# Performance work log

Measured on AMD Instinct MI355X. Metric: run time of the kernel, lower is better.

Reference implementation:

```python
import jax, jax.numpy as jnp
import numpy as np

N_HEADS = 8
NUM_CLASSES = 8
ATTN_INTENSE = 1.0


def setup_inputs() -> dict:
    key = jax.random.key(0)
    k1, k2, k3, k4 = jax.random.split(key, 4)
    bs, width, T = 8, 1536, 1024
    qkv = jax.random.normal(k1, (bs, width, T), dtype=jnp.float32)
    attn_mask = jax.random.randint(k2, (bs, 32, 32), 0, NUM_CLASSES, dtype=jnp.int32)
    # class embedding table: NUM_CLASSES rows + 1 null row (used for the global pass)
    embed_table = jax.random.normal(k3, (NUM_CLASSES + 1, 512), dtype=jnp.float32) * 0.02
    # Conv1d(embed_dim=512 -> 3*ch=192, kernel=1, bias=False) weight
    W_cls = jax.random.normal(k4, (192, 512), dtype=jnp.float32) * 0.02
    return {"qkv": qkv, "attn_mask": attn_mask, "embed_table": embed_table, "W_cls": W_cls}


def _attend(q, k, v, scale):
    # q,k,v: [B, T, C]; returns [B, T, C]
    logits = jnp.einsum('btc,bsc->bts', q * scale, k * scale)
    w = jax.nn.softmax(logits, axis=-1)
    return jnp.einsum('bts,bsc->btc', w, v)


def reference(qkv, attn_mask, embed_table, W_cls):
    bs, width, T = qkv.shape
    H = N_HEADS
    ch = width // (3 * H)            # 64
    scale = ch ** -0.25              # 1/sqrt(sqrt(ch))
    bH = bs * H

    qkv_h = qkv.reshape(bH, 3 * ch, T)
    q = jnp.transpose(qkv_h[:, 0 * ch:1 * ch], (0, 2, 1))  # [bH, T, ch]
    k = jnp.transpose(qkv_h[:, 1 * ch:2 * ch], (0, 2, 1))
    v = jnp.transpose(qkv_h[:, 2 * ch:3 * ch], (0, 2, 1))

    # ---- global pass with null class token ----
    null_tok = W_cls @ embed_table[NUM_CLASSES]  # [3*ch]
    qn, kn, vn = null_tok[:ch], null_tok[ch:2 * ch], null_tok[2 * ch:]
    a = _attend(q + qn, k + kn, v + vn, scale)   # [bH, T, ch]

    # ---- per-region (per segmentation class) attention ----
    seg = attn_mask.reshape(bs, T)
    segs = jnp.repeat(seg, H, axis=0)            # [bH, T], sample-major like qkv reshape

    out = a
    counter = jnp.ones((bH, T), dtype=qkv.dtype)
    for c in range(NUM_CLASSES):
        tok = W_cls @ embed_table[c]             # [3*ch], same token at every region position
        qc, kc, vc = tok[:ch], tok[ch:2 * ch], tok[2 * ch:]
        m = segs == c                            # [bH, T]
        logits = jnp.einsum('btc,bsc->bts', (q + qc) * scale, (k + kc) * scale)
        logits = jnp.where(m[:, None, :], logits, -1e9)   # restrict keys to region
        w = jax.nn.softmax(logits, axis=-1)
        a_c = jnp.einsum('bts,bsc->btc', w, v + vc)
        out = out + jnp.where(m[:, :, None], a_c, 0.0)    # scatter-add onto region queries
        counter = counter + ATTN_INTENSE * m.astype(counter.dtype)

    out = out / counter[:, :, None]              # [bH, T, ch]
    # faithful to original: outs are [ch, T] each, torch.stack(dim=1) -> [ch, bH, T], then reshape
    stacked = jnp.transpose(out, (2, 0, 1))      # [ch, bH, T]
    return stacked.reshape(bs, H * ch, T)
```

## Files before the change

### kernel.cpp

```cpp
#include <hip/hip_runtime.h>
#include <stdint.h>

typedef unsigned short u16;
typedef unsigned int   u32;
typedef __bf16 bf16_t;
typedef bf16_t bf16x8 __attribute__((ext_vector_type(8)));
typedef bf16_t bf16x2 __attribute__((ext_vector_type(2)));
typedef float  f32x2  __attribute__((ext_vector_type(2)));
typedef float  f32x4  __attribute__((ext_vector_type(4)));

#define QSCALE 0.18033688011112042f
#define LP 72

__device__ __forceinline__ u32 pkbf(float a, float b) {
  f32x2 x = {a, b};
  bf16x2 y = __builtin_convertvector(x, bf16x2);
  union { bf16x2 v; u32 u; } c; c.v = y; return c.u;
}

__device__ __forceinline__ float fexp2(float x) {
#if __has_builtin(__builtin_amdgcn_exp2f)
  return __builtin_amdgcn_exp2f(x);
#else
  float r;
  asm("v_exp_f32 %0, %1\n\ts_nop 0" : "=v"(r) : "v"(x));
  return r;
#endif
}

__global__ void tok_kernel(const float* __restrict__ W, const float* __restrict__ E,
                           float* __restrict__ tok) {
  int c = blockIdx.x;
  int j = threadIdx.x;
  const f32x4* wr = (const f32x4*)(W + j * 512);
  const f32x4* er = (const f32x4*)(E + c * 512);
  float acc = 0.f;
  for (int i = 0; i < 128; ++i) {
    f32x4 w = wr[i], e = er[i];
    acc += w.x * e.x + w.y * e.y + w.z * e.z + w.w * e.w;
  }
  tok[c * 192 + j] = acc;
}

__global__ __launch_bounds__(256, 4)
void attn_kernel(const float* __restrict__ qkv, const int* __restrict__ seg,
                 const float* __restrict__ tok, float* __restrict__ out) {
  __shared__ __align__(16) u16 smem[64 * LP * 2 + 4 * 2 * 16 * LP];
  u16* ktr = smem;
  u16* vls = smem + 64 * LP;

  const int L  = blockIdx.x;
  const int bh = (L & 7) * 8 + ((L >> 3) & 7);
  const int qt = L >> 6;
  const int b  = bh >> 3;
  const int tid = threadIdx.x, wave = tid >> 6, lane = tid & 63;
  const int quad = lane >> 4, l16 = lane & 15;
  u16* Pw = smem + 2 * 64 * LP + wave * (2 * 16 * LP);

  const float* qg   = qkv + (size_t)bh * 192 * 1024;
  const int*   segb = seg + b * 1024;

  const int tq = qt * 64 + wave * 16 + l16;
  const int mycls = segb[tq];
  int sq[4];
#pragma unroll
  for (int r = 0; r < 4; ++r) sq[r] = segb[qt * 64 + wave * 16 + quad * 4 + r];

  const float* tn = tok + 8 * 192;
  const float* tc = tok + mycls * 192;
  union { u32 w[4]; bf16x8 v; } q0f[2], qbf[2];
#pragma unroll
  for (int kc = 0; kc < 2; ++kc)
#pragma unroll
    for (int jj = 0; jj < 4; ++jj) {
      int d = kc * 32 + quad * 8 + jj * 2;
      float a0 = qg[(size_t)d * 1024 + tq];
      float a1 = qg[(size_t)(d + 1) * 1024 + tq];
      q0f[kc].w[jj] = pkbf((a0 + tn[d]) * QSCALE, (a1 + tn[d + 1]) * QSCALE);
      qbf[kc].w[jj] = pkbf((a0 + tc[d]) * QSCALE, (a1 + tc[d + 1]) * QSCALE);
    }

  f32x4 O0[4], Ob[4];
#pragma unroll
  for (int dt = 0; dt < 4; ++dt) {
    O0[dt] = (f32x4){0.f, 0.f, 0.f, 0.f};
    Ob[dt] = (f32x4){0.f, 0.f, 0.f, 0.f};
  }
  float rs0[4] = {0.f, 0.f, 0.f, 0.f}, rsb[4] = {0.f, 0.f, 0.f, 0.f};

  const int sK = tid & 63, gK = tid >> 6;
  const int lV = tid & 15, dgV = tid >> 4;
  const float* kbase = qg + (size_t)(64  + gK * 16) * 1024 + sK;
  const float* vbase = qg + (size_t)(128 + dgV * 4) * 1024 + lV;

  for (int kt = 0; kt < 16; ++kt) {
    const int s0 = kt * 64;
    __syncthreads();

    float kf[16];
#pragma unroll
    for (int i = 0; i < 16; ++i) kf[i] = kbase[(size_t)i * 1024 + s0];
    float vf[4][4];
#pragma unroll
    for (int i = 0; i < 4; ++i)
#pragma unroll
      for (int m = 0; m < 4; ++m) vf[i][m] = vbase[(size_t)i * 1024 + s0 + m * 16];

    {
      u32 kp[8];
#pragma unroll
      for (int j = 0; j < 8; ++j) kp[j] = pkbf(kf[2 * j], kf[2 * j + 1]);
      *(uint4*)&ktr[sK * LP + gK * 16]     = make_uint4(kp[0], kp[1], kp[2], kp[3]);
      *(uint4*)&ktr[sK * LP + gK * 16 + 8] = make_uint4(kp[4], kp[5], kp[6], kp[7]);
    }
#pragma unroll
    for (int i = 0; i < 4; ++i)
      *(uint2*)&vls[(dgV * 4 + i) * LP + lV * 4] =
          make_uint2(pkbf(vf[i][0], vf[i][1]), pkbf(vf[i][2], vf[i][3]));

    int sk[4];
#pragma unroll
    for (int n4 = 0; n4 < 4; ++n4) sk[n4] = segb[s0 + n4 * 16 + l16];
    __syncthreads();

    f32x4 S0[4], Sb[4];
#pragma unroll
    for (int n4 = 0; n4 < 4; ++n4) {
      const int scol = n4 * 16 + l16;
      f32x4 a0 = {0.f, 0.f, 0.f, 0.f}, ab = {0.f, 0.f, 0.f, 0.f};
#pragma unroll
      for (int kc = 0; kc < 2; ++kc) {
        bf16x8 kfr = *(const bf16x8*)&ktr[scol * LP + kc * 32 + quad * 8];
        a0 = __builtin_amdgcn_mfma_f32_16x16x32_bf16(q0f[kc].v, kfr, a0, 0, 0, 0);
        ab = __builtin_amdgcn_mfma_f32_16x16x32_bf16(qbf[kc].v, kfr, ab, 0, 0, 0);
      }
      S0[n4] = a0; Sb[n4] = ab;
    }

#pragma unroll
    for (int r = 0; r < 4; ++r) {
      float p0[4], pb[4];
#pragma unroll
      for (int n4 = 0; n4 < 4; ++n4) {
        p0[n4] = fexp2(S0[n4][r]);
        pb[n4] = (sk[n4] == sq[r]) ? fexp2(Sb[n4][r]) : 0.f;
      }
      rs0[r] += (p0[0] + p0[1]) + (p0[2] + p0[3]);
      rsb[r] += (pb[0] + pb[1]) + (pb[2] + pb[3]);
      *(uint2*)&Pw[(quad * 4 + r) * LP + l16 * 4] =
          make_uint2(pkbf(p0[0], p0[1]), pkbf(p0[2], p0[3]));
      *(uint2*)&Pw[16 * LP + (quad * 4 + r) * LP + l16 * 4] =
          make_uint2(pkbf(pb[0], pb[1]), pkbf(pb[2], pb[3]));
    }
    asm volatile("s_waitcnt lgkmcnt(0)" ::: "memory");

#pragma unroll
    for (int kc = 0; kc < 2; ++kc) {
      bf16x8 pf0 = *(const bf16x8*)&Pw[l16 * LP + kc * 32 + quad * 8];
      bf16x8 pfb = *(const bf16x8*)&Pw[16 * LP + l16 * LP + kc * 32 + quad * 8];
#pragma unroll
      for (int dt = 0; dt < 4; ++dt) {
        bf16x8 vfr = *(const bf16x8*)&vls[(dt * 16 + l16) * LP + kc * 32 + quad * 8];
        O0[dt] = __builtin_amdgcn_mfma_f32_16x16x32_bf16(pf0, vfr, O0[dt], 0, 0, 0);
        Ob[dt] = __builtin_amdgcn_mfma_f32_16x16x32_bf16(pfb, vfr, Ob[dt], 0, 0, 0);
      }
    }
  }

#pragma unroll
  for (int r = 0; r < 4; ++r)
#pragma unroll
    for (int off = 1; off < 16; off <<= 1) {
      rs0[r] += __shfl_xor(rs0[r], off, 64);
      rsb[r] += __shfl_xor(rsb[r], off, 64);
    }
  float inv0[4], invb[4];
#pragma unroll
  for (int r = 0; r < 4; ++r) {
    inv0[r] = (rs0[r] > 0.f) ? 1.f / rs0[r] : 0.f;
    invb[r] = (rsb[r] > 0.f) ? 1.f / rsb[r] : 0.f;
  }

  __syncthreads();
  float* fbuf = (float*)smem;
  const float* tvn = tok + 8 * 192 + 128;
#pragma unroll
  for (int dt = 0; dt < 4; ++dt) {
    const int d = dt * 16 + l16;
    const float bn = tvn[d];
#pragma unroll
    for (int r = 0; r < 4; ++r) {
      float bc = tok[sq[r] * 192 + 128 + d];
      float vA = O0[dt][r] * inv0[r] + bn;
      float vB = Ob[dt][r] * invb[r] + bc;
      fbuf[d * 65 + wave * 16 + quad * 4 + r] = 0.5f * (vA + vB);
    }
  }
  __syncthreads();
  {
    const size_t obase = (size_t)bh * 1024 + qt * 64;
    for (int i = tid; i < 4096; i += 256) {
      int d = i >> 6, t = i & 63;
      out[(size_t)d * 65536 + obase + t] = fbuf[d * 65 + t];
    }
  }
}

extern "C" void kernel_launch(void* const* d_in, const int* in_sizes, int n_in,
                              void* d_out, int out_size, void* d_ws, size_t ws_size,
                              hipStream_t stream) {
  (void)in_sizes; (void)n_in; (void)out_size; (void)ws_size;
  const float* qkv   = (const float*)d_in[0];
  const int*   amask = (const int*)d_in[1];
  const float* emb   = (const float*)d_in[2];
  const float* wcls  = (const float*)d_in[3];
  float* tok = (float*)d_ws;
  float* out = (float*)d_out;

  hipLaunchKernelGGL(tok_kernel, dim3(9), dim3(192), 0, stream, wcls, emb, tok);
  hipLaunchKernelGGL(attn_kernel, dim3(1024), dim3(256), 0, stream,
                     qkv, amask, tok, out);
}
```

Baseline: 147.3 us.

## Pre-convert K/V into swizzled bf16 tiles and double-buffer them via async LDS loads

A new prep kernel converts K and V from fp32 to bf16 once per tile and stores them in workspace already laid out with an XOR swizzle. The same launch also computes the class tokens with one wave per output, replacing the old 9-block kernel. The attention kernel now copies each pre-built tile straight into LDS with global_load_lds, double-buffered so the next key tile loads while the current one is computed. This removes the repeated fp32 loads, bf16 conversion and one barrier per iteration, and the swizzle replaces the padded LDS layout. In exchange it adds a 16 MB workspace round-trip, relies on the barrier to wait for the async loads, and lowers the launch-bounds occupancy hint from 4 to 3.

After: 141.2 us. -4.1%, faster.

```diff
diff --git a/kernel.cpp b/kernel.cpp
--- a/kernel.cpp
+++ b/kernel.cpp
@@ -10,7 +10,6 @@
 typedef float  f32x4  __attribute__((ext_vector_type(4)));
 
 #define QSCALE 0.18033688011112042f
-#define LP 72
 
 __device__ __forceinline__ u32 pkbf(float a, float b) {
   f32x2 x = {a, b};
@@ -28,26 +27,75 @@
 #endif
 }
 
-__global__ void tok_kernel(const float* __restrict__ W, const float* __restrict__ E,
-                           float* __restrict__ tok) {
-  int c = blockIdx.x;
-  int j = threadIdx.x;
-  const f32x4* wr = (const f32x4*)(W + j * 512);
-  const f32x4* er = (const f32x4*)(E + c * 512);
-  float acc = 0.f;
-  for (int i = 0; i < 128; ++i) {
-    f32x4 w = wr[i], e = er[i];
-    acc += w.x * e.x + w.y * e.y + w.z * e.z + w.w * e.w;
-  }
-  tok[c * 192 + j] = acc;
-}
-
-__global__ __launch_bounds__(256, 4)
+__device__ __forceinline__ void gload_lds16(const void* g, void* l) {
+  __builtin_amdgcn_global_load_lds(
+      (const __attribute__((address_space(1))) void*)g,
+      (__attribute__((address_space(3))) void*)l, 16, 0, 0);
+}
+
+__global__ __launch_bounds__(256)
+void prep_kernel(const float* __restrict__ qkv,
+                 const float* __restrict__ W, const float* __restrict__ E,
+                 float* __restrict__ tok, u16* __restrict__ tiles) {
+  const int B = blockIdx.x;
+  const int tid = threadIdx.x;
+  if (B >= 1024) {
+    const int gw = (B - 1024) * 4 + (tid >> 6);
+    const int lane = tid & 63;
+    if (gw < 1728) {
+      const int c = gw / 192, j = gw - c * 192;
+      const f32x4* w4 = (const f32x4*)(W + (size_t)j * 512 + lane * 8);
+      const f32x4* e4 = (const f32x4*)(E + (size_t)c * 512 + lane * 8);
+      float acc = 0.f;
+#pragma unroll
+      for (int i = 0; i < 2; ++i) {
+        f32x4 w = w4[i], e = e4[i];
+        acc += w.x * e.x + w.y * e.y + w.z * e.z + w.w * e.w;
+      }
+#pragma unroll
+      for (int off = 32; off; off >>= 1) acc += __shfl_xor(acc, off, 64);
+      if (lane == 0) tok[c * 192 + j] = acc;
+    }
+    return;
+  }
+  const int bh = B >> 4, kt = B & 15;
+  const int s0 = kt * 64;
+  const float* qg = qkv + (size_t)bh * 192 * 1024;
+  u16* img = tiles + (size_t)B * 8192;
+  {
+    const int s = tid & 63, g = tid >> 6;
+    const float* kb = qg + (size_t)(64 + g * 16) * 1024 + s0 + s;
+    float kf[16];
+#pragma unroll
+    for (int i = 0; i < 16; ++i) kf[i] = kb[(size_t)i * 1024];
+    u32 kp[8];
+#pragma unroll
+    for (int j2 = 0; j2 < 8; ++j2) kp[j2] = pkbf(kf[2 * j2], kf[2 * j2 + 1]);
+    const int xr = (s & 7) << 3;
+    *(uint4*)&img[s * 64 + ((g * 16)     ^ xr)] = make_uint4(kp[0], kp[1], kp[2], kp[3]);
+    *(uint4*)&img[s * 64 + ((g * 16 + 8) ^ xr)] = make_uint4(kp[4], kp[5], kp[6], kp[7]);
+  }
+  {
+    const int lV = tid & 15, dg = tid >> 4;
+    const float* vb = qg + (size_t)(128 + dg * 4) * 1024 + s0 + lV;
+#pragma unroll
+    for (int i = 0; i < 4; ++i) {
+      float v0 = vb[(size_t)i * 1024 +  0];
+      float v1 = vb[(size_t)i * 1024 + 16];
+      float v2 = vb[(size_t)i * 1024 + 32];
+      float v3 = vb[(size_t)i * 1024 + 48];
+      const int d = dg * 4 + i;
+      *(uint2*)&img[4096 + d * 64 + ((lV * 4) ^ ((d & 7) << 3))] =
+          make_uint2(pkbf(v0, v1), pkbf(v2, v3));
+    }
+  }
+}
+
+__global__ __launch_bounds__(256, 3)
 void attn_kernel(const float* __restrict__ qkv, const int* __restrict__ seg,
-                 const float* __restrict__ tok, float* __restrict__ out) {
-  __shared__ __align__(16) u16 smem[64 * LP * 2 + 4 * 2 * 16 * LP];
-  u16* ktr = smem;
-  u16* vls = smem + 64 * LP;
+                 const float* __restrict__ tok, const u16* __restrict__ tiles,
+                 float* __restrict__ out) {
+  __shared__ __align__(16) u16 smem[24576];
 
   const int L  = blockIdx.x;
   const int bh = (L & 7) * 8 + ((L >> 3) & 7);
@@ -55,10 +103,11 @@
   const int b  = bh >> 3;
   const int tid = threadIdx.x, wave = tid >> 6, lane = tid & 63;
   const int quad = lane >> 4, l16 = lane & 15;
-  u16* Pw = smem + 2 * 64 * LP + wave * (2 * 16 * LP);
+  u16* Pw = smem + 16384 + wave * 2048;
 
   const float* qg   = qkv + (size_t)bh * 192 * 1024;
   const int*   segb = seg + b * 1024;
+  const u16*   tbh  = tiles + (size_t)bh * (16 * 8192);
 
   const int tq = qt * 64 + wave * 16 + l16;
   const int mycls = segb[tq];
@@ -88,40 +137,31 @@
   }
   float rs0[4] = {0.f, 0.f, 0.f, 0.f}, rsb[4] = {0.f, 0.f, 0.f, 0.f};
 
-  const int sK = tid & 63, gK = tid >> 6;
-  const int lV = tid & 15, dgV = tid >> 4;
-  const float* kbase = qg + (size_t)(64  + gK * 16) * 1024 + sK;
-  const float* vbase = qg + (size_t)(128 + dgV * 4) * 1024 + lV;
-
+  {
+    const char* src = (const char*)tbh + tid * 16;
+    char* dst = (char*)smem + tid * 16;
+#pragma unroll
+    for (int i = 0; i < 4; ++i) gload_lds16(src + i * 4096, dst + i * 4096);
+  }
+
+  const int xq = (l16 & 7) << 3;
+
+#pragma unroll 2
   for (int kt = 0; kt < 16; ++kt) {
     const int s0 = kt * 64;
     __syncthreads();
-
-    float kf[16];
-#pragma unroll
-    for (int i = 0; i < 16; ++i) kf[i] = kbase[(size_t)i * 1024 + s0];
-    float vf[4][4];
-#pragma unroll
-    for (int i = 0; i < 4; ++i)
-#pragma unroll
-      for (int m = 0; m < 4; ++m) vf[i][m] = vbase[(size_t)i * 1024 + s0 + m * 16];
-
-    {
-      u32 kp[8];
-#pragma unroll
-      for (int j = 0; j < 8; ++j) kp[j] = pkbf(kf[2 * j], kf[2 * j + 1]);
-      *(uint4*)&ktr[sK * LP + gK * 16]     = make_uint4(kp[0], kp[1], kp[2], kp[3]);
-      *(uint4*)&ktr[sK * LP + gK * 16 + 8] = make_uint4(kp[4], kp[5], kp[6], kp[7]);
-    }
-#pragma unroll
-    for (int i = 0; i < 4; ++i)
-      *(uint2*)&vls[(dgV * 4 + i) * LP + lV * 4] =
-          make_uint2(pkbf(vf[i][0], vf[i][1]), pkbf(vf[i][2], vf[i][3]));
-
+    if (kt + 1 < 16) {
+      const char* src = (const char*)tbh + (size_t)(kt + 1) * 16384 + tid * 16;
+      char* dst = (char*)smem + ((kt + 1) & 1) * 16384 + tid * 16;
+#pragma unroll
+      for (int i = 0; i < 4; ++i) gload_lds16(src + i * 4096, dst + i * 4096);
+    }
     int sk[4];
 #pragma unroll
     for (int n4 = 0; n4 < 4; ++n4) sk[n4] = segb[s0 + n4 * 16 + l16];
-    __syncthreads();
+
+    const u16* ktr = smem + (kt & 1) * 8192;
+    const u16* vls = ktr + 4096;
 
     f32x4 S0[4], Sb[4];
 #pragma unroll
@@ -130,7 +170,7 @@
       f32x4 a0 = {0.f, 0.f, 0.f, 0.f}, ab = {0.f, 0.f, 0.f, 0.f};
 #pragma unroll
       for (int kc = 0; kc < 2; ++kc) {
-        bf16x8 kfr = *(const bf16x8*)&ktr[scol * LP + kc * 32 + quad * 8];
+        bf16x8 kfr = *(const bf16x8*)&ktr[scol * 64 + ((kc * 32 + quad * 8) ^ xq)];
         a0 = __builtin_amdgcn_mfma_f32_16x16x32_bf16(q0f[kc].v, kfr, a0, 0, 0, 0);
         ab = __builtin_amdgcn_mfma_f32_16x16x32_bf16(qbf[kc].v, kfr, ab, 0, 0, 0);
       }
@@ -139,6 +179,8 @@
 
 #pragma unroll
     for (int r = 0; r < 4; ++r) {
+      const int row = quad * 4 + r;
+      const int po = row * 64 + ((l16 * 4) ^ ((row & 7) << 3));
       float p0[4], pb[4];
 #pragma unroll
       for (int n4 = 0; n4 < 4; ++n4) {
@@ -147,20 +189,19 @@
       }
       rs0[r] += (p0[0] + p0[1]) + (p0[2] + p0[3]);
       rsb[r] += (pb[0] + pb[1]) + (pb[2] + pb[3]);
-      *(uint2*)&Pw[(quad * 4 + r) * LP + l16 * 4] =
-          make_uint2(pkbf(p0[0], p0[1]), pkbf(p0[2], p0[3]));
-      *(uint2*)&Pw[16 * LP + (quad * 4 + r) * LP + l16 * 4] =
-          make_uint2(pkbf(pb[0], pb[1]), pkbf(pb[2], pb[3]));
+      *(uint2*)&Pw[po]        = make_uint2(pkbf(p0[0], p0[1]), pkbf(p0[2], p0[3]));
+      *(uint2*)&Pw[1024 + po] = make_uint2(pkbf(pb[0], pb[1]), pkbf(pb[2], pb[3]));
     }
     asm volatile("s_waitcnt lgkmcnt(0)" ::: "memory");
 
 #pragma unroll
     for (int kc = 0; kc < 2; ++kc) {
-      bf16x8 pf0 = *(const bf16x8*)&Pw[l16 * LP + kc * 32 + quad * 8];
-      bf16x8 pfb = *(const bf16x8*)&Pw[16 * LP + l16 * LP + kc * 32 + quad * 8];
+      const int co = (kc * 32 + quad * 8) ^ xq;
+      bf16x8 pf0 = *(const bf16x8*)&Pw[l16 * 64 + co];
+      bf16x8 pfb = *(const bf16x8*)&Pw[1024 + l16 * 64 + co];
 #pragma unroll
       for (int dt = 0; dt < 4; ++dt) {
-        bf16x8 vfr = *(const bf16x8*)&vls[(dt * 16 + l16) * LP + kc * 32 + quad * 8];
+        bf16x8 vfr = *(const bf16x8*)&vls[(dt * 16 + l16) * 64 + co];
         O0[dt] = __builtin_amdgcn_mfma_f32_16x16x32_bf16(pf0, vfr, O0[dt], 0, 0, 0);
         Ob[dt] = __builtin_amdgcn_mfma_f32_16x16x32_bf16(pfb, vfr, Ob[dt], 0, 0, 0);
       }
@@ -214,10 +255,12 @@
   const int*   amask = (const int*)d_in[1];
   const float* emb   = (const float*)d_in[2];
   const float* wcls  = (const float*)d_in[3];
-  float* tok = (float*)d_ws;
+  float* tok   = (float*)d_ws;
+  u16*   tiles = (u16*)((char*)d_ws + 8192);
   float* out = (float*)d_out;
 
-  hipLaunchKernelGGL(tok_kernel, dim3(9), dim3(192), 0, stream, wcls, emb, tok);
+  hipLaunchKernelGGL(prep_kernel, dim3(1456), dim3(256), 0, stream,
+                     qkv, wcls, emb, tok, tiles);
   hipLaunchKernelGGL(attn_kernel, dim3(1024), dim3(256), 0, stream,
-                     qkv, amask, tok, out);
-}
+                     qkv, amask, tok, tiles, out);
+}
```
